# Kernel optimization log

Hardware: AMD Instinct MI355X
Metric: run time of the kernel (lower is better)

## Reference

```python
import jax, jax.numpy as jnp
import numpy as np

EMB_DIM = 1024
D_K = 64
B, S = 4, 4096

def setup_inputs() -> dict:
    key = jax.random.key(0)
    ks = jax.random.split(key, 8)
    inv = 1.0 / np.sqrt(EMB_DIM)
    return {
        "input1": jax.random.normal(ks[0], (B, S, EMB_DIM), dtype=jnp.float32),
        "input2": jax.random.normal(ks[1], (B, S, EMB_DIM), dtype=jnp.float32),
        "Wq": jax.random.uniform(ks[2], (EMB_DIM, D_K), jnp.float32, -inv, inv),
        "bq": jax.random.uniform(ks[3], (D_K,), jnp.float32, -inv, inv),
        "Wk": jax.random.uniform(ks[4], (EMB_DIM, D_K), jnp.float32, -inv, inv),
        "bk": jax.random.uniform(ks[5], (D_K,), jnp.float32, -inv, inv),
        "Wv": jax.random.uniform(ks[6], (EMB_DIM, D_K), jnp.float32, -inv, inv),
        "bv": jax.random.uniform(ks[7], (D_K,), jnp.float32, -inv, inv),
    }

def reference(input1, input2, Wq, bq, Wk, bk, Wv, bv):
    # queries from input2; keys/values from input1 (as in the torch forward)
    q = input2 @ Wq + bq            # [B, Sq, d_k]
    k = input1 @ Wk + bk            # [B, Sk, d_k]
    v = input1 @ Wv + bv            # [B, Sk, d_k]
    scale = 1.0 / jnp.sqrt(jnp.asarray(D_K, q.dtype))
    scores = jnp.einsum("bqd,bkd->bqk", q, k) * scale  # [B, Sq, Sk]
    attn = jax.nn.softmax(scores, axis=-1)
    return jnp.einsum("bqk,bkd->bqd", attn, v)          # [B, Sq, d_k]
```

## Files before the change

### kernel.cpp

```cpp
#include <hip/hip_runtime.h>
#include <hip/hip_bf16.h>

#define E 1024
#define DK 64
#define SEQ 4096
#define NB 4
#define KSCALE 0.125f
#define AROW 68

typedef short bf16x8 __attribute__((ext_vector_type(8)));
typedef short bf16x4 __attribute__((ext_vector_type(4)));
typedef float f32x4 __attribute__((ext_vector_type(4)));

typedef const __attribute__((address_space(1))) unsigned int* gcp;
typedef __attribute__((address_space(3))) unsigned int* lcp;

__device__ inline unsigned short f2bf(float f) {
    unsigned int u = __float_as_uint(f);
    u += 0x7fff + ((u >> 16) & 1);
    return (unsigned short)(u >> 16);
}

__global__ __launch_bounds__(256) void wt_kernel(
    const float* __restrict__ Wq, const float* __restrict__ Wk, const float* __restrict__ Wv,
    unsigned short* __restrict__ wtq, unsigned short* __restrict__ wtk, unsigned short* __restrict__ wtv)
{
    const float* src; unsigned short* dst;
    if (blockIdx.y == 0)      { src = Wq; dst = wtq; }
    else if (blockIdx.y == 1) { src = Wk; dst = wtk; }
    else                      { src = Wv; dst = wtv; }
    const int tid = threadIdx.x;
    const int e0 = blockIdx.x * 64;
    __shared__ float Ws[64][65];
    #pragma unroll
    for (int i = 0; i < 4; ++i) {
        int flat = i * 256 + tid;
        int r = flat >> 4;
        int c4 = (flat & 15) << 2;
        float4 v = *reinterpret_cast<const float4*>(&src[(size_t)(e0 + r) * DK + c4]);
        Ws[c4 + 0][r] = v.x; Ws[c4 + 1][r] = v.y; Ws[c4 + 2][r] = v.z; Ws[c4 + 3][r] = v.w;
    }
    __syncthreads();
    #pragma unroll
    for (int i = 0; i < 4; ++i) {
        int flat = i * 256 + tid;
        int c = flat >> 4;
        int r4 = (flat & 15) << 2;
        ushort4 o;
        o.x = f2bf(Ws[c][r4 + 0]); o.y = f2bf(Ws[c][r4 + 1]);
        o.z = f2bf(Ws[c][r4 + 2]); o.w = f2bf(Ws[c][r4 + 3]);
        *reinterpret_cast<ushort4*>(&dst[(size_t)c * E + e0 + r4]) = o;
    }
}

__global__ __launch_bounds__(256, 2) void proj_kernel(
    const float* __restrict__ in_q, const float* __restrict__ in_kv,
    const unsigned short* __restrict__ wtq, const unsigned short* __restrict__ wtk,
    const unsigned short* __restrict__ wtv,
    const float* __restrict__ bq, const float* __restrict__ bk, const float* __restrict__ bv,
    unsigned short* __restrict__ Qw, unsigned short* __restrict__ Kw, unsigned short* __restrict__ Vtw)
{
    const int tid = threadIdx.x;
    const int w = tid >> 6, lane = tid & 63, quad = lane >> 4, l16 = lane & 15;
    const int row0 = blockIdx.x * 64;
    const bool isQ = (blockIdx.y == 0);
    const float* A = isQ ? in_q : in_kv;
    const unsigned short* w0 = isQ ? wtq : wtk;

    __shared__ float As[2][64 * AROW];
    __shared__ unsigned short W0s[2][64 * 64];
    __shared__ unsigned short W1s[2][64 * 64];

    const int rl = lane >> 3, pp = lane & 7;

    {
        #pragma unroll
        for (int i = 0; i < 16; ++i) {
            int r = w * 16 + i;
            const float* src = A + (size_t)(row0 + r) * E + lane;
            __builtin_amdgcn_global_load_lds((gcp)(const void*)src, (lcp)(void*)&As[0][r * AROW], 4, 0, 0);
        }
        #pragma unroll
        for (int i = 0; i < 2; ++i) {
            int g = w * 2 + i;
            int r = g * 8 + rl;
            int lc = pp ^ (r & 7);
            __builtin_amdgcn_global_load_lds((gcp)(const void*)(w0 + (size_t)r * E + lc * 8),
                                             (lcp)(void*)&W0s[0][g * 512], 16, 0, 0);
            if (!isQ)
                __builtin_amdgcn_global_load_lds((gcp)(const void*)(wtv + (size_t)r * E + lc * 8),
                                                 (lcp)(void*)&W1s[0][g * 512], 16, 0, 0);
        }
    }
    __syncthreads();

    f32x4 acc0[4] = {};
    f32x4 acc1[4] = {};

    #pragma unroll 2
    for (int kb = 0; kb < 16; ++kb) {
        const int cur = kb & 1, nxt = cur ^ 1;
        const bool pf = (kb < 15);
        if (pf) {
            const int ko = (kb + 1) * 64;
            #pragma unroll
            for (int i = 0; i < 16; ++i) {
                int r = w * 16 + i;
                const float* src = A + (size_t)(row0 + r) * E + ko + lane;
                __builtin_amdgcn_global_load_lds((gcp)(const void*)src, (lcp)(void*)&As[nxt][r * AROW], 4, 0, 0);
            }
            #pragma unroll
            for (int i = 0; i < 2; ++i) {
                int g = w * 2 + i;
                int r = g * 8 + rl;
                int lc = pp ^ (r & 7);
                __builtin_amdgcn_global_load_lds((gcp)(const void*)(w0 + (size_t)r * E + ko + lc * 8),
                                                 (lcp)(void*)&W0s[nxt][g * 512], 16, 0, 0);
                if (!isQ)
                    __builtin_amdgcn_global_load_lds((gcp)(const void*)(wtv + (size_t)r * E + ko + lc * 8),
                                                     (lcp)(void*)&W1s[nxt][g * 512], 16, 0, 0);
            }
        }
        const int arow = w * 16 + l16;
        #pragma unroll
        for (int ks = 0; ks < 2; ++ks) {
            const float* ap = &As[cur][arow * AROW + ks * 32 + quad * 8];
            f32x4 a0 = *reinterpret_cast<const f32x4*>(ap);
            f32x4 a1 = *reinterpret_cast<const f32x4*>(ap + 4);
            bf16x8 af = { (short)f2bf(a0[0]), (short)f2bf(a0[1]), (short)f2bf(a0[2]), (short)f2bf(a0[3]),
                          (short)f2bf(a1[0]), (short)f2bf(a1[1]), (short)f2bf(a1[2]), (short)f2bf(a1[3]) };
            #pragma unroll
            for (int ct = 0; ct < 4; ++ct) {
                int brow = ct * 16 + l16;
                int pc = (ks * 4 + quad) ^ (brow & 7);
                bf16x8 b0 = *reinterpret_cast<const bf16x8*>(&W0s[cur][brow * 64 + pc * 8]);
                acc0[ct] = __builtin_amdgcn_mfma_f32_16x16x32_bf16(af, b0, acc0[ct], 0, 0, 0);
                if (!isQ) {
                    bf16x8 b1 = *reinterpret_cast<const bf16x8*>(&W1s[cur][brow * 64 + pc * 8]);
                    acc1[ct] = __builtin_amdgcn_mfma_f32_16x16x32_bf16(af, b1, acc1[ct], 0, 0, 0);
                }
            }
        }
        if (pf) __syncthreads();
    }

    const int orow0 = row0 + w * 16 + quad * 4;
    #pragma unroll
    for (int ct = 0; ct < 4; ++ct) {
        int col = ct * 16 + l16;
        if (isQ) {
            float bias = bq[col];
            #pragma unroll
            for (int r = 0; r < 4; ++r)
                Qw[(size_t)(orow0 + r) * DK + col] = f2bf(acc0[ct][r] + bias);
        } else {
            float biask = bk[col], biasv = bv[col];
            #pragma unroll
            for (int r = 0; r < 4; ++r) {
                int grow = orow0 + r;
                Kw[(size_t)grow * DK + col] = f2bf((acc0[ct][r] + biask) * KSCALE);
                int bb = grow >> 12;
                int tok = grow & 4095;
                Vtw[((size_t)(bb * 64 + col)) * SEQ + tok] = f2bf(acc1[ct][r] + biasv);
            }
        }
    }
}

__global__ __launch_bounds__(256) void attn_kernel(
    const unsigned short* __restrict__ Qw, const unsigned short* __restrict__ Kw,
    const unsigned short* __restrict__ Vtw, float* __restrict__ out)
{
    const int tid = threadIdx.x;
    const int w = tid >> 6, lane = tid & 63, quad = lane >> 4, l16 = lane & 15;
    const int qt = blockIdx.x & 63;
    const int b = blockIdx.x >> 6;

    __shared__ unsigned short Ks[2][64 * 64];
    __shared__ unsigned short Vts[2][64 * 64];
    __shared__ float LDSf[4][16][68];
    __shared__ float LDSl[4][4][16];

    bf16x8 qfb[2][4];
    #pragma unroll
    for (int ks = 0; ks < 2; ++ks)
        #pragma unroll
        for (int ct = 0; ct < 4; ++ct)
            qfb[ks][ct] = *reinterpret_cast<const bf16x8*>(
                &Qw[((size_t)(b * SEQ + qt * 64 + ct * 16 + l16)) * DK + ks * 32 + quad * 8]);

    const int rl = lane >> 3, pp = lane & 7;

    #pragma unroll
    for (int i = 0; i < 2; ++i) {
        int g = w * 2 + i;
        int r = g * 8 + rl;
        int lc = pp ^ (r & 7);
        __builtin_amdgcn_global_load_lds((gcp)(const void*)&Kw[((size_t)(b * SEQ + r)) * DK + lc * 8],
                                         (lcp)(void*)&Ks[0][g * 512], 16, 0, 0);
        __builtin_amdgcn_global_load_lds((gcp)(const void*)&Vtw[((size_t)(b * 64 + r)) * SEQ + lc * 8],
                                         (lcp)(void*)&Vts[0][g * 512], 16, 0, 0);
    }
    __syncthreads();

    float lp[4] = {0.f, 0.f, 0.f, 0.f};
    f32x4 o[4][4] = {};

    #pragma unroll 2
    for (int kt = 0; kt < 64; ++kt) {
        const int cur = kt & 1, nxt = cur ^ 1;
        const bool pf = (kt < 63);
        if (pf) {
            const int gk = (kt + 1) * 64;
            #pragma unroll
            for (int i = 0; i < 2; ++i) {
                int g = w * 2 + i;
                int r = g * 8 + rl;
                int lc = pp ^ (r & 7);
                __builtin_amdgcn_global_load_lds((gcp)(const void*)&Kw[((size_t)(b * SEQ + gk + r)) * DK + lc * 8],
                                                 (lcp)(void*)&Ks[nxt][g * 512], 16, 0, 0);
                __builtin_amdgcn_global_load_lds((gcp)(const void*)&Vtw[((size_t)(b * 64 + r)) * SEQ + gk + lc * 8],
                                                 (lcp)(void*)&Vts[nxt][g * 512], 16, 0, 0);
            }
        }

        const int krow = w * 16 + l16;
        bf16x8 kf0 = *reinterpret_cast<const bf16x8*>(&Ks[cur][krow * 64 + ((quad) ^ (krow & 7)) * 8]);
        bf16x8 kf1 = *reinterpret_cast<const bf16x8*>(&Ks[cur][krow * 64 + ((4 + quad) ^ (krow & 7)) * 8]);

        f32x4 sacc[4] = {};
        #pragma unroll
        for (int ct = 0; ct < 4; ++ct) {
            sacc[ct] = __builtin_amdgcn_mfma_f32_16x16x32_bf16(kf0, qfb[0][ct], sacc[ct], 0, 0, 0);
            sacc[ct] = __builtin_amdgcn_mfma_f32_16x16x32_bf16(kf1, qfb[1][ct], sacc[ct], 0, 0, 0);
        }

        bf16x4 va[4];
        #pragma unroll
        for (int ct = 0; ct < 4; ++ct) {
            int vrow = ct * 16 + l16;
            int pc = (w * 2 + (quad >> 1)) ^ (vrow & 7);
            va[ct] = *reinterpret_cast<const bf16x4*>(&Vts[cur][vrow * 64 + pc * 8 + (quad & 1) * 4]);
        }

        #pragma unroll
        for (int cq = 0; cq < 4; ++cq) {
            float p0 = __expf(sacc[cq][0]);
            float p1 = __expf(sacc[cq][1]);
            float p2 = __expf(sacc[cq][2]);
            float p3 = __expf(sacc[cq][3]);
            lp[cq] += (p0 + p1) + (p2 + p3);
            bf16x4 pb = { (short)f2bf(p0), (short)f2bf(p1), (short)f2bf(p2), (short)f2bf(p3) };
            #pragma unroll
            for (int cd = 0; cd < 4; ++cd)
                o[cd][cq] = __builtin_amdgcn_mfma_f32_16x16x16bf16_1k(va[cd], pb, o[cd][cq], 0, 0, 0);
        }

        if (pf) __syncthreads();
    }

    #pragma unroll
    for (int cq = 0; cq < 4; ++cq) {
        float t = lp[cq];
        t += __shfl_xor(t, 16, 64);
        t += __shfl_xor(t, 32, 64);
        lp[cq] = t;
    }
    if (lane < 16)
        #pragma unroll
        for (int cq = 0; cq < 4; ++cq)
            LDSl[w][cq][lane] = lp[cq];

    const int ql = tid >> 4, d4 = (tid & 15) << 2;
    #pragma unroll
    for (int cq = 0; cq < 4; ++cq) {
        #pragma unroll
        for (int cd = 0; cd < 4; ++cd)
            *reinterpret_cast<f32x4*>(&LDSf[w][l16][cd * 16 + quad * 4]) = o[cd][cq];
        __syncthreads();
        f32x4 acc = {};
        #pragma unroll
        for (int w2 = 0; w2 < 4; ++w2)
            acc += *reinterpret_cast<const f32x4*>(&LDSf[w2][ql][d4]);
        float lq = LDSl[0][cq][ql] + LDSl[1][cq][ql] + LDSl[2][cq][ql] + LDSl[3][cq][ql];
        f32x4 res = acc * (1.0f / lq);
        *reinterpret_cast<f32x4*>(&out[((size_t)(b * SEQ + qt * 64 + cq * 16 + ql)) * DK + d4]) = res;
        __syncthreads();
    }
}

extern "C" void kernel_launch(void* const* d_in, const int* in_sizes, int n_in,
                              void* d_out, int out_size, void* d_ws, size_t ws_size,
                              hipStream_t stream) {
    const float* input1 = (const float*)d_in[0];
    const float* input2 = (const float*)d_in[1];
    const float* Wq = (const float*)d_in[2];
    const float* bq = (const float*)d_in[3];
    const float* Wk = (const float*)d_in[4];
    const float* bk = (const float*)d_in[5];
    const float* Wv = (const float*)d_in[6];
    const float* bv = (const float*)d_in[7];
    float* out = (float*)d_out;

    char* ws = (char*)d_ws;
    unsigned short* wtq = (unsigned short*)(ws + 0);
    unsigned short* wtk = (unsigned short*)(ws + 131072);
    unsigned short* wtv = (unsigned short*)(ws + 262144);
    unsigned short* Qw  = (unsigned short*)(ws + 393216);
    unsigned short* Kw  = (unsigned short*)(ws + 2490368);
    unsigned short* Vtw = (unsigned short*)(ws + 4587520);

    wt_kernel<<<dim3(16, 3), 256, 0, stream>>>(Wq, Wk, Wv, wtq, wtk, wtv);
    proj_kernel<<<dim3(256, 2), 256, 0, stream>>>(input2, input1, wtq, wtk, wtv,
                                                  bq, bk, bv, Qw, Kw, Vtw);
    attn_kernel<<<dim3(256), 256, 0, stream>>>(Qw, Kw, Vtw, out);
}
```

Baseline: 229.2 us.

## Use per-wave triple-buffered K/V staging in attention and vectorize projection loads

The attention kernel now gives each wave its own private K and V^T slices in LDS, since every wave only ever reads its own 16 keys. It triple-buffers those slices with a two-tile prefetch and drops the block-wide __syncthreads. Block indices are remapped so neighbouring blocks interleave batches and query tiles, which may change L2 reuse. The projection kernel replaces 4-byte LDS-DMA loads of the fp32 activations with 16-byte loads into an XOR-swizzled unpadded tile, cutting load instruction count. The risk is that without explicit barriers, correctness and overlap depend on the compiler inserting the right vmcnt waits for the async LDS loads.

```diff
diff --git a/kernel.cpp b/kernel.cpp
--- a/kernel.cpp
+++ b/kernel.cpp
@@ -6,7 +6,6 @@
 #define SEQ 4096
 #define NB 4
 #define KSCALE 0.125f
-#define AROW 68
 
 typedef short bf16x8 __attribute__((ext_vector_type(8)));
 typedef short bf16x4 __attribute__((ext_vector_type(4)));
@@ -67,18 +66,21 @@
     const float* A = isQ ? in_q : in_kv;
     const unsigned short* w0 = isQ ? wtq : wtk;
 
-    __shared__ float As[2][64 * AROW];
+    __shared__ float As[2][64 * 64];
     __shared__ unsigned short W0s[2][64 * 64];
     __shared__ unsigned short W1s[2][64 * 64];
 
+    const int ar = (lane >> 4);
+    const int ap = lane & 15;
     const int rl = lane >> 3, pp = lane & 7;
 
     {
         #pragma unroll
-        for (int i = 0; i < 16; ++i) {
-            int r = w * 16 + i;
-            const float* src = A + (size_t)(row0 + r) * E + lane;
-            __builtin_amdgcn_global_load_lds((gcp)(const void*)src, (lcp)(void*)&As[0][r * AROW], 4, 0, 0);
+        for (int i = 0; i < 4; ++i) {
+            int r = w * 16 + i * 4 + ar;
+            int lc = ap ^ (2 * (r & 7));
+            __builtin_amdgcn_global_load_lds((gcp)(const void*)(A + (size_t)(row0 + r) * E + lc * 4),
+                                             (lcp)(void*)&As[0][(w * 16 + i * 4) * 64], 16, 0, 0);
         }
         #pragma unroll
         for (int i = 0; i < 2; ++i) {
@@ -104,10 +106,11 @@
         if (pf) {
             const int ko = (kb + 1) * 64;
             #pragma unroll
-            for (int i = 0; i < 16; ++i) {
-                int r = w * 16 + i;
-                const float* src = A + (size_t)(row0 + r) * E + ko + lane;
-                __builtin_amdgcn_global_load_lds((gcp)(const void*)src, (lcp)(void*)&As[nxt][r * AROW], 4, 0, 0);
+            for (int i = 0; i < 4; ++i) {
+                int r = w * 16 + i * 4 + ar;
+                int lc = ap ^ (2 * (r & 7));
+                __builtin_amdgcn_global_load_lds((gcp)(const void*)(A + (size_t)(row0 + r) * E + ko + lc * 4),
+                                                 (lcp)(void*)&As[nxt][(w * 16 + i * 4) * 64], 16, 0, 0);
             }
             #pragma unroll
             for (int i = 0; i < 2; ++i) {
@@ -122,11 +125,13 @@
             }
         }
         const int arow = w * 16 + l16;
+        const int am = 2 * (arow & 7);
         #pragma unroll
         for (int ks = 0; ks < 2; ++ks) {
-            const float* ap = &As[cur][arow * AROW + ks * 32 + quad * 8];
-            f32x4 a0 = *reinterpret_cast<const f32x4*>(ap);
-            f32x4 a1 = *reinterpret_cast<const f32x4*>(ap + 4);
+            int q0c = (2 * (ks * 4 + quad)) ^ am;
+            const float* apt = &As[cur][arow * 64 + q0c * 4];
+            f32x4 a0 = *reinterpret_cast<const f32x4*>(apt);
+            f32x4 a1 = *reinterpret_cast<const f32x4*>(apt + 4);
             bf16x8 af = { (short)f2bf(a0[0]), (short)f2bf(a0[1]), (short)f2bf(a0[2]), (short)f2bf(a0[3]),
                           (short)f2bf(a1[0]), (short)f2bf(a1[1]), (short)f2bf(a1[2]), (short)f2bf(a1[3]) };
             #pragma unroll
@@ -173,11 +178,11 @@
 {
     const int tid = threadIdx.x;
     const int w = tid >> 6, lane = tid & 63, quad = lane >> 4, l16 = lane & 15;
-    const int qt = blockIdx.x & 63;
-    const int b = blockIdx.x >> 6;
-
-    __shared__ unsigned short Ks[2][64 * 64];
-    __shared__ unsigned short Vts[2][64 * 64];
+    const int b = (blockIdx.x & 7) >> 1;
+    const int qt = ((blockIdx.x >> 3) << 1) | (blockIdx.x & 1);
+
+    __shared__ unsigned short Kbuf[4][3][1024];
+    __shared__ unsigned short Vbuf[4][3][1024];
     __shared__ float LDSf[4][16][68];
     __shared__ float LDSl[4][4][16];
 
@@ -189,44 +194,44 @@
             qfb[ks][ct] = *reinterpret_cast<const bf16x8*>(
                 &Qw[((size_t)(b * SEQ + qt * 64 + ct * 16 + l16)) * DK + ks * 32 + quad * 8]);
 
-    const int rl = lane >> 3, pp = lane & 7;
-
-    #pragma unroll
-    for (int i = 0; i < 2; ++i) {
-        int g = w * 2 + i;
-        int r = g * 8 + rl;
-        int lc = pp ^ (r & 7);
-        __builtin_amdgcn_global_load_lds((gcp)(const void*)&Kw[((size_t)(b * SEQ + r)) * DK + lc * 8],
-                                         (lcp)(void*)&Ks[0][g * 512], 16, 0, 0);
-        __builtin_amdgcn_global_load_lds((gcp)(const void*)&Vtw[((size_t)(b * 64 + r)) * SEQ + lc * 8],
-                                         (lcp)(void*)&Vts[0][g * 512], 16, 0, 0);
-    }
-    __syncthreads();
+    const int kr = lane >> 3, kc = lane & 7;
+    const int vr = lane >> 1, vh = lane & 1;
+
+    const unsigned short* Kbase = Kw + (size_t)(b * SEQ) * DK + w * 16 * DK;
+    const unsigned short* Vbase = Vtw + (size_t)(b * 64) * SEQ + w * 16;
+
+    auto stage = [&](int kt, int st) {
+        const unsigned short* kp = Kbase + (size_t)kt * 64 * DK;
+        #pragma unroll
+        for (int i = 0; i < 2; ++i) {
+            int r = i * 8 + kr;
+            int lc = kc ^ (r & 7);
+            __builtin_amdgcn_global_load_lds((gcp)(const void*)(kp + (size_t)r * DK + lc * 8),
+                                             (lcp)(void*)&Kbuf[w][st][i * 512], 16, 0, 0);
+        }
+        const unsigned short* vp = Vbase + (size_t)kt * 64;
+        #pragma unroll
+        for (int i = 0; i < 2; ++i) {
+            int r = i * 32 + vr;
+            __builtin_amdgcn_global_load_lds((gcp)(const void*)(vp + (size_t)r * SEQ + vh * 8),
+                                             (lcp)(void*)&Vbuf[w][st][i * 512], 16, 0, 0);
+        }
+    };
+
+    stage(0, 0);
+    stage(1, 1);
 
     float lp[4] = {0.f, 0.f, 0.f, 0.f};
     f32x4 o[4][4] = {};
 
-    #pragma unroll 2
+    const int km = l16 & 7;
+    #pragma unroll 1
     for (int kt = 0; kt < 64; ++kt) {
-        const int cur = kt & 1, nxt = cur ^ 1;
-        const bool pf = (kt < 63);
-        if (pf) {
-            const int gk = (kt + 1) * 64;
-            #pragma unroll
-            for (int i = 0; i < 2; ++i) {
-                int g = w * 2 + i;
-                int r = g * 8 + rl;
-                int lc = pp ^ (r & 7);
-                __builtin_amdgcn_global_load_lds((gcp)(const void*)&Kw[((size_t)(b * SEQ + gk + r)) * DK + lc * 8],
-                                                 (lcp)(void*)&Ks[nxt][g * 512], 16, 0, 0);
-                __builtin_amdgcn_global_load_lds((gcp)(const void*)&Vtw[((size_t)(b * 64 + r)) * SEQ + gk + lc * 8],
-                                                 (lcp)(void*)&Vts[nxt][g * 512], 16, 0, 0);
-            }
-        }
-
-        const int krow = w * 16 + l16;
-        bf16x8 kf0 = *reinterpret_cast<const bf16x8*>(&Ks[cur][krow * 64 + ((quad) ^ (krow & 7)) * 8]);
-        bf16x8 kf1 = *reinterpret_cast<const bf16x8*>(&Ks[cur][krow * 64 + ((4 + quad) ^ (krow & 7)) * 8]);
+        const int cur = kt % 3;
+        if (kt + 2 < 64) stage(kt + 2, (kt + 2) % 3);
+
+        bf16x8 kf0 = *reinterpret_cast<const bf16x8*>(&Kbuf[w][cur][l16 * 64 + ((quad ^ km) * 8)]);
+        bf16x8 kf1 = *reinterpret_cast<const bf16x8*>(&Kbuf[w][cur][l16 * 64 + (((quad ^ km) ^ 4) * 8)]);
 
         f32x4 sacc[4] = {};
         #pragma unroll
@@ -237,11 +242,8 @@
 
         bf16x4 va[4];
         #pragma unroll
-        for (int ct = 0; ct < 4; ++ct) {
-            int vrow = ct * 16 + l16;
-            int pc = (w * 2 + (quad >> 1)) ^ (vrow & 7);
-            va[ct] = *reinterpret_cast<const bf16x4*>(&Vts[cur][vrow * 64 + pc * 8 + (quad & 1) * 4]);
-        }
+        for (int ct = 0; ct < 4; ++ct)
+            va[ct] = *reinterpret_cast<const bf16x4*>(&Vbuf[w][cur][(ct * 16 + l16) * 16 + quad * 4]);
 
         #pragma unroll
         for (int cq = 0; cq < 4; ++cq) {
@@ -255,8 +257,6 @@
             for (int cd = 0; cd < 4; ++cd)
                 o[cd][cq] = __builtin_amdgcn_mfma_f32_16x16x16bf16_1k(va[cd], pb, o[cd][cq], 0, 0, 0);
         }
-
-        if (pf) __syncthreads();
     }
 
     #pragma unroll
```

New measurement: 228.4 us. Within noise of the previous version (-0.3%).
